# Kernel tuning notes

Measured on AMD Instinct MI355X. Metric: run time of the kernel, lower is better.

The kernel has to match this reference:

```python
import jax, jax.numpy as jnp
import numpy as np

N, F, K = 2048, 256, 4
E = 65536

def setup_inputs() -> dict:
    key = jax.random.key(0)
    ks = jax.random.split(key, 8)
    batch_x = jax.random.normal(ks[0], (N, F), dtype=jnp.float32)
    # eigen-matrix of a normalized Laplacian is diagonal in practice, but the
    # original code treats it as a dense [N,N] operand; we mimic a diagonal
    # eigenvalue matrix (eigenvalues in [0,2]) -- math is identical either way.
    lam_diag = 2.0 * jax.random.uniform(ks[1], (N,), dtype=jnp.float32)
    batch_lam = jnp.diag(lam_diag)
    batch_U = jax.random.normal(ks[2], (N, N), dtype=jnp.float32) / jnp.sqrt(jnp.float32(N))
    # init.uniform_(a, 0, 2) / (b, 0, 2) / (c, -1, 1); keep a-b bounded away from 0
    a_list = 1.0 + jax.random.uniform(ks[3], (K,), dtype=jnp.float32)        # [1,2)
    b_list = 0.9 * jax.random.uniform(ks[4], (K,), dtype=jnp.float32)       # [0,0.9)
    c_list = 2.0 * jax.random.uniform(ks[5], (K,), dtype=jnp.float32) - 1.0  # [-1,1)
    residual_alpha = jnp.ones((1,), dtype=jnp.float32)
    edge_index = jax.random.randint(ks[6], (2, E), 0, N, dtype=jnp.int64)
    return {"batch_x": batch_x, "batch_lam": batch_lam, "batch_U": batch_U,
            "a_list": a_list, "b_list": b_list, "c_list": c_list,
            "residual_alpha": residual_alpha, "edge_index": edge_index}

def reference(batch_x, batch_lam, batch_U, a_list, b_list, c_list, residual_alpha, edge_index):
    n = batch_lam.shape[0]
    I = jnp.eye(n, dtype=batch_lam.dtype)
    out = residual_alpha * batch_x  # residual added at hop 0 in original
    for i in range(a_list.shape[0]):
        # filter_rep = (a_i*I - Lam) @ (Lam - b_i*I), then relu
        rep = (a_list[i] * I - batch_lam) @ (batch_lam - b_list[i] * I)
        rep = jax.nn.relu(rep)
        scale = c_list[i] / ((a_list[i] - b_list[i]) * (a_list[i] - b_list[i]) / 4.0)
        filt = scale * (batch_U @ (rep @ (batch_U.T @ batch_x)))
        out = out + filt
    return out
```

## Files before the change

### kernel.cpp

```cpp
#include <hip/hip_runtime.h>
#include <type_traits>

typedef unsigned short u16;
typedef __attribute__((ext_vector_type(8))) short short8;
typedef __attribute__((ext_vector_type(4))) float floatx4;

__device__ __forceinline__ u16 f2u(float f) {
  unsigned int x = __float_as_uint(f);
  x += 0x7fff + ((x >> 16) & 1);
  return (u16)(x >> 16);
}

__device__ __forceinline__ void async16(const void* g, void* l) {
  __builtin_amdgcn_global_load_lds(
      (const __attribute__((address_space(1))) unsigned int*)g,
      (__attribute__((address_space(3))) unsigned int*)l, 16, 0, 0);
}

__global__ __launch_bounds__(256) void prep_kernel(
    const float* __restrict__ U, const float* __restrict__ x,
    const float* __restrict__ lam, const float* __restrict__ a,
    const float* __restrict__ b, const float* __restrict__ c,
    u16* __restrict__ Ut, u16* __restrict__ Ubf, u16* __restrict__ xT,
    float* __restrict__ dvec, int N, int F) {
  __shared__ __attribute__((aligned(16))) float tile[64][65];
  int bb = blockIdx.x;
  int t = threadIdx.x;

  if (bb >= 1152) {
    int j = (bb - 1152) * 256 + t;
    float lv = lam[(size_t)j * N + j];
    float acc = 0.f;
#pragma unroll
    for (int i = 0; i < 4; ++i) {
      float ai = a[i], bi = b[i], ci = c[i];
      float rep = (ai - lv) * (lv - bi);
      rep = rep > 0.f ? rep : 0.f;
      acc += ci * 4.f / ((ai - bi) * (ai - bi)) * rep;
    }
    dvec[j] = acc;
    return;
  }

  const float* in;
  u16 *outT, *outC;
  int R, C, c0, r0;
  if (bb < 1024) {
    in = U; outT = Ut; outC = Ubf; R = N; C = N;
    c0 = (bb & 31) * 64; r0 = (bb >> 5) * 64;
  } else {
    int b2 = bb - 1024;
    in = x; outT = xT; outC = nullptr; R = N; C = F;
    c0 = (b2 & 3) * 64; r0 = (b2 >> 2) * 64;
  }

#pragma unroll
  for (int p = 0; p < 4; ++p) {
    int e = p * 256 + t;
    int row = e >> 4, col = (e & 15) * 4;
    float4 v = *(const float4*)(in + (size_t)(r0 + row) * C + c0 + col);
    tile[row][col] = v.x;
    tile[row][col + 1] = v.y;
    tile[row][col + 2] = v.z;
    tile[row][col + 3] = v.w;
    if (outC) {
      union { uint2 u; u16 s[4]; } pk;
      pk.s[0] = f2u(v.x); pk.s[1] = f2u(v.y);
      pk.s[2] = f2u(v.z); pk.s[3] = f2u(v.w);
      *(uint2*)(outC + (size_t)(r0 + row) * C + c0 + col) = pk.u;
    }
  }
  __syncthreads();
#pragma unroll
  for (int p = 0; p < 2; ++p) {
    int e = p * 256 + t;
    int orow = e >> 3, oc = (e & 7) * 8;
    union { uint4 v; u16 s[8]; } tmp;
#pragma unroll
    for (int i = 0; i < 8; ++i) tmp.s[i] = f2u(tile[oc + i][orow]);
    *(uint4*)(outT + (size_t)(c0 + orow) * R + r0 + oc) = tmp.v;
  }
}

template <bool SCALE_D, bool RESIDUAL, typename CT>
__global__ __launch_bounds__(256) void gemm_tn(
    const u16* __restrict__ A, const u16* __restrict__ B, CT* __restrict__ C,
    int M, int NN, int K, const float* __restrict__ dvec,
    const float* __restrict__ resid, const float* __restrict__ alpha_p) {
  __shared__ __attribute__((aligned(16))) u16 lA[2 * 4 * 64 * 32];
  __shared__ __attribute__((aligned(16))) u16 lB[2 * 4 * 32 * 32];
  const int m0 = blockIdx.x * 64;
  const int n0 = blockIdx.y * 32;
  const int t = threadIdx.x;
  const int wave = t >> 6;
  const int lane = t & 63;
  const int wm = wave >> 1, wn = wave & 1;
  const int q = lane >> 4, l15 = lane & 15;

  const u16* gA = A + (size_t)(m0 + (t >> 2)) * K + (t & 3) * 8;
  const u16* gB = B + (size_t)(n0 + ((t & 127) >> 2)) * K + (t & 3) * 8;
  char* lAc = (char*)lA;
  char* lBc = (char*)lB;

  const int NM = K >> 7;

  auto issue = [&](int i, int buf) {
#pragma unroll
    for (int st = 0; st < 4; ++st)
      async16(gA + i * 128 + st * 32, lAc + buf * 16384 + st * 4096 + t * 16);
    if (t < 128) {
#pragma unroll
      for (int st = 0; st < 4; ++st)
        async16(gB + i * 128 + st * 32, lBc + buf * 8192 + st * 2048 + t * 16);
    }
  };

  floatx4 acc[2];
  acc[0] = (floatx4){0.f, 0.f, 0.f, 0.f};
  acc[1] = (floatx4){0.f, 0.f, 0.f, 0.f};

  issue(0, 0);
  for (int i = 0; i < NM; ++i) {
    const int buf = i & 1;
    __syncthreads();
    if (i + 1 < NM) issue(i + 1, buf ^ 1);
    const u16* lAb = lA + buf * 8192;
    const u16* lBb = lB + buf * 4096;
#pragma unroll
    for (int st = 0; st < 4; ++st) {
      short8 a0 = *(const short8*)&lAb[st * 2048 + (wm * 32 + l15) * 32 + q * 8];
      short8 a1 = *(const short8*)&lAb[st * 2048 + (wm * 32 + 16 + l15) * 32 + q * 8];
      short8 bf = *(const short8*)&lBb[st * 1024 + (wn * 16 + l15) * 32 + q * 8];
      acc[0] = __builtin_amdgcn_mfma_f32_16x16x32_bf16(a0, bf, acc[0], 0, 0, 0);
      acc[1] = __builtin_amdgcn_mfma_f32_16x16x32_bf16(a1, bf, acc[1], 0, 0, 0);
    }
  }

  float alpha = 0.f;
  if (RESIDUAL) alpha = alpha_p[0];
  const int col = n0 + wn * 16 + l15;
  float ds = 1.f;
  if (SCALE_D) ds = dvec[col];
#pragma unroll
  for (int mt = 0; mt < 2; ++mt) {
    int rbase = m0 + wm * 32 + mt * 16 + q * 4;
#pragma unroll
    for (int r = 0; r < 4; ++r) {
      float v = acc[mt][r];
      if (SCALE_D) v *= ds;
      size_t idx = (size_t)(rbase + r) * NN + col;
      if (RESIDUAL) v += alpha * resid[idx];
      if constexpr (std::is_same<CT, u16>::value)
        C[idx] = f2u(v);
      else
        C[idx] = v;
    }
  }
}

extern "C" void kernel_launch(void* const* d_in, const int* in_sizes, int n_in,
                              void* d_out, int out_size, void* d_ws,
                              size_t ws_size, hipStream_t stream) {
  const int N = 2048, F = 256;
  const float* x = (const float*)d_in[0];
  const float* lam = (const float*)d_in[1];
  const float* U = (const float*)d_in[2];
  const float* a = (const float*)d_in[3];
  const float* b = (const float*)d_in[4];
  const float* c = (const float*)d_in[5];
  const float* alpha = (const float*)d_in[6];

  char* ws = (char*)d_ws;
  float* dvec = (float*)ws;
  u16* xT = (u16*)(ws + 8192);
  u16* Ut = (u16*)(ws + 8192 + (1 << 20));
  u16* Ubf = (u16*)(ws + 8192 + (9 << 20));
  u16* zT = (u16*)(ws + 8192 + (17 << 20));

  prep_kernel<<<1160, 256, 0, stream>>>(U, x, lam, a, b, c, Ut, Ubf, xT,
                                        dvec, N, F);
  gemm_tn<true, false, u16><<<dim3(F / 64, N / 32), 256, 0, stream>>>(
      xT, Ut, zT, F, N, N, dvec, nullptr, nullptr);
  gemm_tn<false, true, float><<<dim3(N / 64, F / 32), 256, 0, stream>>>(
      Ubf, zT, (float*)d_out, N, F, N, nullptr, x, alpha);
}
```

Before: 119.2 us.

## Shrink GEMM tiles to 32x32 and fuse filter-diagonal computation into epilogue

Halves the M tile of both GEMMs so each launches twice as many blocks, giving more waves per CU on a grid that previously had roughly one block per CU. The per-column filter scale is now computed directly in the first GEMM's epilogue from lambda and the coefficients, removing the dvec blocks from the prep kernel and the workspace vector. Smaller tiles reduce data reuse per block and raise global/LDS traffic per MFMA, and the diagonal scale is recomputed redundantly per thread.

After: 114.2 us. -4.3%, faster.

```diff
diff --git a/kernel.cpp b/kernel.cpp
--- a/kernel.cpp
+++ b/kernel.cpp
@@ -19,28 +19,11 @@
 
 __global__ __launch_bounds__(256) void prep_kernel(
     const float* __restrict__ U, const float* __restrict__ x,
-    const float* __restrict__ lam, const float* __restrict__ a,
-    const float* __restrict__ b, const float* __restrict__ c,
     u16* __restrict__ Ut, u16* __restrict__ Ubf, u16* __restrict__ xT,
-    float* __restrict__ dvec, int N, int F) {
+    int N, int F) {
   __shared__ __attribute__((aligned(16))) float tile[64][65];
   int bb = blockIdx.x;
   int t = threadIdx.x;
-
-  if (bb >= 1152) {
-    int j = (bb - 1152) * 256 + t;
-    float lv = lam[(size_t)j * N + j];
-    float acc = 0.f;
-#pragma unroll
-    for (int i = 0; i < 4; ++i) {
-      float ai = a[i], bi = b[i], ci = c[i];
-      float rep = (ai - lv) * (lv - bi);
-      rep = rep > 0.f ? rep : 0.f;
-      acc += ci * 4.f / ((ai - bi) * (ai - bi)) * rep;
-    }
-    dvec[j] = acc;
-    return;
-  }
 
   const float* in;
   u16 *outT, *outC;
@@ -83,78 +66,81 @@
 }
 
 template <bool SCALE_D, bool RESIDUAL, typename CT>
-__global__ __launch_bounds__(256) void gemm_tn(
+__global__ __launch_bounds__(256) void gemm32(
     const u16* __restrict__ A, const u16* __restrict__ B, CT* __restrict__ C,
-    int M, int NN, int K, const float* __restrict__ dvec,
-    const float* __restrict__ resid, const float* __restrict__ alpha_p) {
-  __shared__ __attribute__((aligned(16))) u16 lA[2 * 4 * 64 * 32];
+    int M, int NN, int K, const float* __restrict__ lam,
+    const float* __restrict__ pa, const float* __restrict__ pb,
+    const float* __restrict__ pc, const float* __restrict__ resid,
+    const float* __restrict__ alpha_p) {
+  __shared__ __attribute__((aligned(16))) u16 lA[2 * 4 * 32 * 32];
   __shared__ __attribute__((aligned(16))) u16 lB[2 * 4 * 32 * 32];
-  const int m0 = blockIdx.x * 64;
+  const int m0 = blockIdx.x * 32;
   const int n0 = blockIdx.y * 32;
   const int t = threadIdx.x;
-  const int wave = t >> 6;
-  const int lane = t & 63;
+  const int wave = t >> 6, lane = t & 63;
   const int wm = wave >> 1, wn = wave & 1;
   const int q = lane >> 4, l15 = lane & 15;
 
-  const u16* gA = A + (size_t)(m0 + (t >> 2)) * K + (t & 3) * 8;
-  const u16* gB = B + (size_t)(n0 + ((t & 127) >> 2)) * K + (t & 3) * 8;
+  const int within = t & 127, st0 = t >> 7;
+  const u16* gA = A + (size_t)(m0 + (within >> 2)) * K + (within & 3) * 8;
+  const u16* gB = B + (size_t)(n0 + (within >> 2)) * K + (within & 3) * 8;
   char* lAc = (char*)lA;
   char* lBc = (char*)lB;
 
   const int NM = K >> 7;
 
   auto issue = [&](int i, int buf) {
-#pragma unroll
-    for (int st = 0; st < 4; ++st)
-      async16(gA + i * 128 + st * 32, lAc + buf * 16384 + st * 4096 + t * 16);
-    if (t < 128) {
-#pragma unroll
-      for (int st = 0; st < 4; ++st)
-        async16(gB + i * 128 + st * 32, lBc + buf * 8192 + st * 2048 + t * 16);
-    }
+    int k0 = i * 128;
+    async16(gA + k0 + st0 * 32, lAc + buf * 8192 + t * 16);
+    async16(gA + k0 + (st0 + 2) * 32, lAc + buf * 8192 + 4096 + t * 16);
+    async16(gB + k0 + st0 * 32, lBc + buf * 8192 + t * 16);
+    async16(gB + k0 + (st0 + 2) * 32, lBc + buf * 8192 + 4096 + t * 16);
   };
 
-  floatx4 acc[2];
-  acc[0] = (floatx4){0.f, 0.f, 0.f, 0.f};
-  acc[1] = (floatx4){0.f, 0.f, 0.f, 0.f};
+  floatx4 acc = (floatx4){0.f, 0.f, 0.f, 0.f};
 
   issue(0, 0);
   for (int i = 0; i < NM; ++i) {
     const int buf = i & 1;
     __syncthreads();
     if (i + 1 < NM) issue(i + 1, buf ^ 1);
-    const u16* lAb = lA + buf * 8192;
+    const u16* lAb = lA + buf * 4096;
     const u16* lBb = lB + buf * 4096;
 #pragma unroll
     for (int st = 0; st < 4; ++st) {
-      short8 a0 = *(const short8*)&lAb[st * 2048 + (wm * 32 + l15) * 32 + q * 8];
-      short8 a1 = *(const short8*)&lAb[st * 2048 + (wm * 32 + 16 + l15) * 32 + q * 8];
+      short8 af = *(const short8*)&lAb[st * 1024 + (wm * 16 + l15) * 32 + q * 8];
       short8 bf = *(const short8*)&lBb[st * 1024 + (wn * 16 + l15) * 32 + q * 8];
-      acc[0] = __builtin_amdgcn_mfma_f32_16x16x32_bf16(a0, bf, acc[0], 0, 0, 0);
-      acc[1] = __builtin_amdgcn_mfma_f32_16x16x32_bf16(a1, bf, acc[1], 0, 0, 0);
+      acc = __builtin_amdgcn_mfma_f32_16x16x32_bf16(af, bf, acc, 0, 0, 0);
     }
   }
 
+  const int col = n0 + wn * 16 + l15;
+  float ds = 1.f;
+  if (SCALE_D) {
+    float lv = lam[(size_t)col * NN + col];
+    float dacc = 0.f;
+#pragma unroll
+    for (int i = 0; i < 4; ++i) {
+      float ai = pa[i], bi = pb[i], ci = pc[i];
+      float rep = (ai - lv) * (lv - bi);
+      rep = rep > 0.f ? rep : 0.f;
+      dacc += ci * 4.f / ((ai - bi) * (ai - bi)) * rep;
+    }
+    ds = dacc;
+  }
   float alpha = 0.f;
   if (RESIDUAL) alpha = alpha_p[0];
-  const int col = n0 + wn * 16 + l15;
-  float ds = 1.f;
-  if (SCALE_D) ds = dvec[col];
+  const int rbase = m0 + wm * 16 + q * 4;
 #pragma unroll
-  for (int mt = 0; mt < 2; ++mt) {
-    int rbase = m0 + wm * 32 + mt * 16 + q * 4;
-#pragma unroll
-    for (int r = 0; r < 4; ++r) {
-      float v = acc[mt][r];
-      if (SCALE_D) v *= ds;
-      size_t idx = (size_t)(rbase + r) * NN + col;
-      if (RESIDUAL) v += alpha * resid[idx];
-      if constexpr (std::is_same<CT, u16>::value)
-        C[idx] = f2u(v);
-      else
-        C[idx] = v;
-    }
+  for (int r = 0; r < 4; ++r) {
+    float v = acc[r];
+    if (SCALE_D) v *= ds;
+    size_t idx = (size_t)(rbase + r) * NN + col;
+    if (RESIDUAL) v += alpha * resid[idx];
+    if constexpr (std::is_same<CT, u16>::value)
+      C[idx] = f2u(v);
+    else
+      C[idx] = v;
   }
 }
 
@@ -171,16 +157,15 @@
   const float* alpha = (const float*)d_in[6];
 
   char* ws = (char*)d_ws;
-  float* dvec = (float*)ws;
-  u16* xT = (u16*)(ws + 8192);
-  u16* Ut = (u16*)(ws + 8192 + (1 << 20));
-  u16* Ubf = (u16*)(ws + 8192 + (9 << 20));
-  u16* zT = (u16*)(ws + 8192 + (17 << 20));
+  u16* xT = (u16*)ws;
+  u16* Ut = (u16*)(ws + (1 << 20));
+  u16* Ubf = (u16*)(ws + (9 << 20));
+  u16* zT = (u16*)(ws + (17 << 20));
 
-  prep_kernel<<<1160, 256, 0, stream>>>(U, x, lam, a, b, c, Ut, Ubf, xT,
-                                        dvec, N, F);
-  gemm_tn<true, false, u16><<<dim3(F / 64, N / 32), 256, 0, stream>>>(
-      xT, Ut, zT, F, N, N, dvec, nullptr, nullptr);
-  gemm_tn<false, true, float><<<dim3(N / 64, F / 32), 256, 0, stream>>>(
-      Ubf, zT, (float*)d_out, N, F, N, nullptr, x, alpha);
+  prep_kernel<<<1152, 256, 0, stream>>>(U, x, Ut, Ubf, xT, N, F);
+  gemm32<true, false, u16><<<dim3(F / 32, N / 32), 256, 0, stream>>>(
+      xT, Ut, zT, F, N, N, lam, a, b, c, nullptr, nullptr);
+  gemm32<false, true, float><<<dim3(N / 32, F / 32), 256, 0, stream>>>(
+      Ubf, zT, (float*)d_out, N, F, N, nullptr, nullptr, nullptr, nullptr,
+      x, alpha);
 }
```
